# Kernel tuning notes

Hardware: AMD Instinct MI355X
Metric: run time of the kernel (lower is better)

Reference implementation:

```python
import jax, jax.numpy as jnp
import numpy as np
from jax import lax

B, C_IN, H, W = 32, 2048, 14, 14
C_MID = 1024
EPS = 1e-5


def _bn(x, gamma, beta, mean, var):
    # eval-mode batchnorm over channel axis 1 of NCHW
    inv = gamma / jnp.sqrt(var + EPS)
    return x * inv[None, :, None, None] + (beta - mean * inv)[None, :, None, None]


def setup_inputs() -> dict:
    key = jax.random.key(0)
    ks = jax.random.split(key, 16)
    x = jax.random.normal(ks[0], (B, C_IN, H, W), jnp.float32)
    # conv1: 3x3, 2048 -> 1024, xavier-normal init
    std1 = np.sqrt(2.0 / (C_IN * 9 + C_MID * 9)).astype(np.float32)
    w1 = jax.random.normal(ks[1], (C_MID, C_IN, 3, 3), jnp.float32) * std1
    b1 = jnp.zeros((C_MID,), jnp.float32)
    bn1_gamma = 1.0 + 0.1 * jax.random.normal(ks[2], (C_MID,), jnp.float32)
    bn1_beta = 0.1 * jax.random.normal(ks[3], (C_MID,), jnp.float32)
    bn1_mean = 0.1 * jax.random.normal(ks[4], (C_MID,), jnp.float32)
    bn1_var = jax.random.uniform(ks[5], (C_MID,), jnp.float32, 0.5, 1.5)
    # selectLayer: 1x1, 1024 -> 18 (stored as [out, in])
    std_s = np.sqrt(2.0 / (C_MID + 18)).astype(np.float32)
    w_sel = jax.random.normal(ks[6], (18, C_MID), jnp.float32) * std_s
    b_sel = jnp.zeros((18,), jnp.float32)
    # boxLayer: 1x1, 1024 -> 36, uniform(-5, 5) init
    w_box = jax.random.uniform(ks[7], (36, C_MID), jnp.float32, -5.0, 5.0)
    b_box = jnp.zeros((36,), jnp.float32)
    bnb_gamma = 1.0 + 0.1 * jax.random.normal(ks[8], (36,), jnp.float32)
    bnb_beta = 0.1 * jax.random.normal(ks[9], (36,), jnp.float32)
    bnb_mean = 0.1 * jax.random.normal(ks[10], (36,), jnp.float32)
    bnb_var = jax.random.uniform(ks[11], (36,), jnp.float32, 0.5, 1.5)
    return {
        'x': x, 'w1': w1, 'b1': b1,
        'bn1_gamma': bn1_gamma, 'bn1_beta': bn1_beta, 'bn1_mean': bn1_mean, 'bn1_var': bn1_var,
        'w_sel': w_sel, 'b_sel': b_sel,
        'w_box': w_box, 'b_box': b_box,
        'bnb_gamma': bnb_gamma, 'bnb_beta': bnb_beta, 'bnb_mean': bnb_mean, 'bnb_var': bnb_var,
    }


def reference(x, w1, b1, bn1_gamma, bn1_beta, bn1_mean, bn1_var,
              w_sel, b_sel, w_box, b_box,
              bnb_gamma, bnb_beta, bnb_mean, bnb_var):
    n = x.shape[0]
    # conv1 + BN + ReLU (3x3, padding=1)
    h = lax.conv_general_dilated(x, w1, (1, 1), 'SAME',
                                 dimension_numbers=('NCHW', 'OIHW', 'NCHW'))
    h = h + b1[None, :, None, None]
    h = jax.nn.relu(_bn(h, bn1_gamma, bn1_beta, bn1_mean, bn1_var))
    # selectLayer: 1x1 conv + ReLU -> [n, 18, H, W]
    score = jnp.einsum('nchw,oc->nohw', h, w_sel) + b_sel[None, :, None, None]
    score = jax.nn.relu(score)
    # boxLayer: 1x1 conv + BN + ReLU -> [n, 36, H, W]
    box = jnp.einsum('nchw,oc->nohw', h, w_box) + b_box[None, :, None, None]
    box = jax.nn.relu(_bn(box, bnb_gamma, bnb_beta, bnb_mean, bnb_var))
    # permute NCHW -> NHWC, reshape to anchors
    box = jnp.transpose(box, (0, 2, 3, 1)).reshape(n, -1, 4) * 419.0  # [n, 1764, 4]
    score = jnp.transpose(score, (0, 2, 3, 1)).reshape(n, -1, 2)      # [n, 1764, 2]
    score = jax.nn.softmax(score, axis=-1)
    return score, box
```

## Files before the change

kernel.cpp:

```cpp
#include <hip/hip_runtime.h>
#include <hip/hip_bf16.h>
#include <math.h>

#define CIN   2048
#define CMID  1024
#define NB    32
#define HWSP  196
#define NPOS  6272
#define WELEM 2097152
#define NST64 144

typedef __attribute__((ext_vector_type(4))) float f32x4;
typedef __attribute__((ext_vector_type(8))) short short8;
typedef __attribute__((ext_vector_type(4))) float float4v;

typedef const __attribute__((address_space(1))) unsigned int* as1_u32p;
typedef __attribute__((address_space(3))) unsigned int* as3_u32p;

__device__ __forceinline__ void gload_lds16(const void* g, void* l) {
  __builtin_amdgcn_global_load_lds((as1_u32p)g, (as3_u32p)l, 16, 0, 0);
}

__global__ __launch_bounds__(256) void pack_w(
    const float* __restrict__ w1, const float* __restrict__ b1,
    const float* __restrict__ g1, const float* __restrict__ be1,
    const float* __restrict__ mu1, const float* __restrict__ va1,
    const float* __restrict__ wsel, const float* __restrict__ wbox,
    __hip_bfloat16* __restrict__ Wp, float* __restrict__ inv1,
    float* __restrict__ add1, float* __restrict__ Wh)
{
  __shared__ float lw[2304];
  const int gid0 = blockIdx.x * 256;
  const float4v* src4 = (const float4v*)(w1 + (long)gid0 * 9);
  float4v* l4 = (float4v*)lw;
  #pragma unroll
  for (int i = 0; i < 3; ++i) {
    int idx = i * 256 + threadIdx.x;
    if (idx < 576) l4[idx] = src4[idx];
  }
  __syncthreads();
  const int gid = gid0 + threadIdx.x;
  float v[9];
  #pragma unroll
  for (int k = 0; k < 9; ++k) v[k] = lw[threadIdx.x * 9 + k];
  #pragma unroll
  for (int k = 0; k < 9; ++k)
    Wp[(long)k * WELEM + gid] = __float2bfloat16(v[k]);

  if (gid < CMID) {
    float iv = g1[gid] / sqrtf(va1[gid] + 1e-5f);
    inv1[gid] = iv;
    add1[gid] = b1[gid] * iv + be1[gid] - mu1[gid] * iv;
  }
  if (gid < CMID * 54) {
    int co = gid / 54, o = gid % 54;
    Wh[gid] = (o < 18) ? wsel[o * CMID + co] : wbox[(o - 18) * CMID + co];
  }
}

__global__ __launch_bounds__(256) void pack_x(
    const float* __restrict__ x, __hip_bfloat16* __restrict__ Xp)
{
  __shared__ __hip_bfloat16 lx[64 * HWSP];
  const int n = blockIdx.x;
  const int cc = blockIdx.y;
  const int ci0 = cc * 64;
  const float* src = x + ((long)n * CIN + ci0) * HWSP;
  for (int i = threadIdx.x; i < 64 * HWSP; i += 256)
    lx[i] = __float2bfloat16(src[i]);
  __syncthreads();
  const int ci = threadIdx.x & 63;
  const int pq = threadIdx.x >> 6;
  __hip_bfloat16* dst = Xp + (long)n * 256 * CIN + ci0 + ci;
  const __hip_bfloat16 z = __float2bfloat16(0.f);
  #pragma unroll
  for (int k = 0; k < 64; ++k) {
    int pos = k * 4 + pq;
    int y = pos >> 4, xx = pos & 15;
    __hip_bfloat16 v = z;
    if (y >= 1 && y <= 14 && xx >= 1 && xx <= 14)
      v = lx[ci * HWSP + (y - 1) * 14 + (xx - 1)];
    dst[(long)pos * CIN] = v;
  }
}

__global__ __launch_bounds__(256, 2) void conv_mfma(
    const __hip_bfloat16* __restrict__ Wp,
    const __hip_bfloat16* __restrict__ Xp,
    __hip_bfloat16* __restrict__ hout0,
    __hip_bfloat16* __restrict__ hout1)
{
  __shared__ char smem[2 * 32768];

  const int t = threadIdx.x;
  const int bx = blockIdx.x;
  const int r  = bx & 7;
  const int q  = bx >> 3;
  const int kidx = q >> 3;
  int mtile = q & 7;
  int ntile;
  if (kidx < 6) {
    ntile = r + 8 * kidx;
  } else {
    if (r != (q & 7)) return;
    ntile = 48;
  }
  const int z = blockIdx.y;
  const int lane = t & 63;
  const int wv = t >> 6;
  const int wr2 = wv >> 1;
  const int wc2 = wv & 1;

  const int srow = t >> 2;
  const int swb = ((t & 3) << 4) ^ ((srow & 6) << 3);

  const long arowbase = (long)(mtile * 128 + srow) * CIN + (swb >> 1);

  long bbase[2];
  #pragma unroll
  for (int i = 0; i < 2; ++i) {
    int jj = ntile * 128 + srow + 64 * i;
    int n0 = jj / HWSP, p0 = jj % HWSP;
    int hh = p0 / 14, ww = p0 % 14;
    bbase[i] = (long)(n0 * 256 + hh * 16 + ww) * CIN + (swb >> 1);
  }

  const int fr = lane & 15;
  const int ksl = lane >> 4;
  const int kgsw = ((ksl << 4) ^ ((fr & 6) << 3));

  f32x4 acc[4][4] = {};
  short8 a_[4], b_[4];

  const int g0 = z * NST64;

  #define STAGE_A(gv, bi) do {                                                  \
    int g_ = (gv);                                                              \
    int kt_ = g_ >> 5;                                                          \
    int ck_ = (g_ & 31) << 6;                                                   \
    char* d_ = smem + (bi) * 32768;                                             \
    const __hip_bfloat16* ap_ = Wp + (long)kt_ * WELEM + arowbase + ck_;        \
    _Pragma("unroll")                                                           \
    for (int h_ = 0; h_ < 2; ++h_)                                              \
      _Pragma("unroll")                                                         \
      for (int i_ = 0; i_ < 2; ++i_)                                            \
        gload_lds16(ap_ + h_ * 32 + (long)i_ * 64 * CIN,                        \
                    d_ + h_ * 8192 + i_ * 4096 + t * 16);                       \
  } while (0)

  #define STAGE_B(gv, bi) do {                                                  \
    int g_ = (gv);                                                              \
    int kt_ = g_ >> 5;                                                          \
    int ck_ = (g_ & 31) << 6;                                                   \
    int kh_ = (kt_ * 11) >> 5;                                                  \
    int kw_ = kt_ - kh_ * 3;                                                    \
    char* d_ = smem + (bi) * 32768 + 16384;                                     \
    long boff_ = (long)(kh_ * 16 + kw_) * CIN + ck_;                            \
    _Pragma("unroll")                                                           \
    for (int h_ = 0; h_ < 2; ++h_)                                              \
      _Pragma("unroll")                                                         \
      for (int i_ = 0; i_ < 2; ++i_)                                            \
        gload_lds16(Xp + bbase[i_] + boff_ + h_ * 32,                           \
                    d_ + h_ * 8192 + i_ * 4096 + t * 16);                       \
  } while (0)

  #define READ_H(bi, h) do {                                                    \
    const char* cb_ = smem + (bi) * 32768 + (h) * 8192;                         \
    _Pragma("unroll")                                                           \
    for (int i = 0; i < 4; ++i)                                                 \
      a_[i] = *(const short8*)(cb_ + (wr2 * 64 + i * 16 + fr) * 64 + kgsw);     \
    _Pragma("unroll")                                                           \
    for (int i = 0; i < 4; ++i)                                                 \
      b_[i] = *(const short8*)(cb_ + 16384 + (wc2 * 64 + i * 16 + fr) * 64 + kgsw); \
  } while (0)

  #define MFMA_H() do {                                                         \
    __builtin_amdgcn_s_setprio(1);                                              \
    _Pragma("unroll")                                                           \
    for (int m = 0; m < 4; ++m)                                                 \
      _Pragma("unroll")                                                         \
      for (int n = 0; n < 4; ++n)                                               \
        acc[m][n] = __builtin_amdgcn_mfma_f32_16x16x32_bf16(a_[m], b_[n], acc[m][n], 0, 0, 0); \
    __builtin_amdgcn_s_setprio(0);                                              \
  } while (0)

  #define WAITV4() asm volatile("s_waitcnt vmcnt(4)" ::: "memory")
  #define WAITV0() asm volatile("s_waitcnt vmcnt(0)" ::: "memory")
  #define BAR() do { asm volatile("" ::: "memory");                             \
                     __builtin_amdgcn_s_barrier();                              \
                     asm volatile("" ::: "memory"); } while (0)

  STAGE_A(g0 + 0, 0);
  STAGE_B(g0 + 0, 0);

  for (int s = 0; s < NST64 - 1; ++s) {
    const int c = s & 1, n = c ^ 1;
    STAGE_A(g0 + s + 1, n);
    WAITV4();
    BAR();
    READ_H(c, 0);
    MFMA_H();
    STAGE_B(g0 + s + 1, n);
    READ_H(c, 1);
    BAR();
    MFMA_H();
  }
  {
    const int c = (NST64 - 1) & 1;
    WAITV0(); BAR();
    READ_H(c, 0);
    MFMA_H();
    READ_H(c, 1);
    MFMA_H();
  }

  __hip_bfloat16* dsth = z ? hout1 : hout0;
  const int rg = ksl * 4;
  #pragma unroll
  for (int m = 0; m < 4; ++m) {
    const int co0 = mtile * 128 + wr2 * 64 + m * 16 + rg;
    #pragma unroll
    for (int r_ = 0; r_ < 4; ++r_) {
      const int co = co0 + r_;
      #pragma unroll
      for (int n = 0; n < 4; ++n) {
        const int j = ntile * 128 + wc2 * 64 + n * 16 + fr;
        dsth[(long)co * NPOS + j] = __float2bfloat16(acc[m][n][r_]);
      }
    }
  }
  #undef STAGE_A
  #undef STAGE_B
  #undef READ_H
  #undef MFMA_H
  #undef WAITV4
  #undef WAITV0
  #undef BAR
}

__global__ __launch_bounds__(256) void head_fused(
    const __hip_bfloat16* __restrict__ h0, const __hip_bfloat16* __restrict__ h1,
    const float* __restrict__ Wh,
    const float* __restrict__ inv1, const float* __restrict__ add1,
    const float* __restrict__ bsel, const float* __restrict__ bbox,
    const float* __restrict__ gb, const float* __restrict__ beb,
    const float* __restrict__ mub, const float* __restrict__ vab,
    float* __restrict__ out)
{
  __shared__ float red[4 * 64 * 54];
  const int t = threadIdx.x;
  const int jl = t & 63;
  const int cg = __builtin_amdgcn_readfirstlane(t >> 6);
  const int j0 = blockIdx.x * 64;
  const int j = j0 + jl;

  float acc[54];
  #pragma unroll
  for (int o = 0; o < 54; ++o) acc[o] = 0.f;

  const __hip_bfloat16* hp0 = h0 + (long)(cg * 256) * NPOS + j;
  const __hip_bfloat16* hp1 = h1 + (long)(cg * 256) * NPOS + j;
  const float* wp = Wh + cg * 256 * 54;
  const float* ivp = inv1 + cg * 256;
  const float* adp = add1 + cg * 256;
  for (int i = 0; i < 256; ++i) {
    float hv = __bfloat162float(hp0[(long)i * NPOS]) + __bfloat162float(hp1[(long)i * NPOS]);
    hv = fmaxf(hv * ivp[i] + adp[i], 0.f);
    const float* wr_ = wp + i * 54;
    #pragma unroll
    for (int o = 0; o < 54; ++o) acc[o] += hv * wr_[o];
  }
  #pragma unroll
  for (int o = 0; o < 54; ++o) red[(cg * 64 + jl) * 54 + o] = acc[o];
  __syncthreads();

  for (int idx = t; idx < 576; idx += 256) {
    int jj = idx / 9, pr = idx % 9;
    float s0 = bsel[2 * pr], s1 = bsel[2 * pr + 1];
    #pragma unroll
    for (int c = 0; c < 4; ++c) {
      s0 += red[(c * 64 + jj) * 54 + 2 * pr];
      s1 += red[(c * 64 + jj) * 54 + 2 * pr + 1];
    }
    s0 = fmaxf(s0, 0.f); s1 = fmaxf(s1, 0.f);
    float mx = fmaxf(s0, s1);
    float e0 = expf(s0 - mx), e1 = expf(s1 - mx);
    float inv = 1.f / (e0 + e1);
    int jg = j0 + jj;
    int nn = jg / HWSP, p = jg % HWSP;
    long off = ((long)nn * 1764 + p * 9 + pr) * 2;
    out[off] = e0 * inv;
    out[off + 1] = e1 * inv;
  }

  float* outb = out + (long)NB * 1764 * 2;
  for (int idx = t; idx < 2304; idx += 256) {
    int jj = idx / 36, o = idx % 36;
    float v = bbox[o];
    #pragma unroll
    for (int c = 0; c < 4; ++c) v += red[(c * 64 + jj) * 54 + 18 + o];
    float iv = gb[o] / sqrtf(vab[o] + 1e-5f);
    v = v * iv + (beb[o] - mub[o] * iv);
    v = fmaxf(v, 0.f) * 419.f;
    int jg = j0 + jj;
    int nn = jg / HWSP, p = jg % HWSP;
    outb[((long)nn * 1764 + p * 9 + (o >> 2)) * 4 + (o & 3)] = v;
  }
}

extern "C" void kernel_launch(void* const* d_in, const int* in_sizes, int n_in,
                              void* d_out, int out_size, void* d_ws, size_t ws_size,
                              hipStream_t stream) {
  const float* x    = (const float*)d_in[0];
  const float* w1   = (const float*)d_in[1];
  const float* b1   = (const float*)d_in[2];
  const float* g1   = (const float*)d_in[3];
  const float* be1  = (const float*)d_in[4];
  const float* mu1  = (const float*)d_in[5];
  const float* va1  = (const float*)d_in[6];
  const float* wsel = (const float*)d_in[7];
  const float* bsel = (const float*)d_in[8];
  const float* wbox = (const float*)d_in[9];
  const float* bbox = (const float*)d_in[10];
  const float* gb   = (const float*)d_in[11];
  const float* beb  = (const float*)d_in[12];
  const float* mub  = (const float*)d_in[13];
  const float* vab  = (const float*)d_in[14];

  char* ws = (char*)d_ws;
  __hip_bfloat16* Wp = (__hip_bfloat16*)(ws);
  __hip_bfloat16* Xp = (__hip_bfloat16*)(ws + 37748736);
  __hip_bfloat16* hb0 = (__hip_bfloat16*)(ws + 71303168);
  __hip_bfloat16* hb1 = (__hip_bfloat16*)(ws + 84148224);
  float* inv1        = (float*)(ws + 96993280);
  float* add1        = (float*)(ws + 96997376);
  float* Wh          = (float*)(ws + 97001472);

  hipLaunchKernelGGL(pack_w, dim3(8192), dim3(256), 0, stream,
                     w1, b1, g1, be1, mu1, va1, wsel, wbox, Wp, inv1, add1, Wh);
  hipLaunchKernelGGL(pack_x, dim3(32, 32), dim3(256), 0, stream, x, Xp);
  hipLaunchKernelGGL(conv_mfma, dim3(448, 2), dim3(256), 0, stream,
                     Wp, Xp, hb0, hb1);
  hipLaunchKernelGGL(head_fused, dim3(98), dim3(256), 0, stream,
                     hb0, hb1, Wh, inv1, add1, bsel, bbox, gb, beb, mub, vab, (float*)d_out);
}
```

Before: 403.2 us.

## Merge weight and input pack kernels; read both K-halves from LDS before MFMAs

Combines pack_w and pack_x into one launch that dispatches on block index, removing a kernel launch and the gap between the two packing passes. In the conv main loop, both halves of the LDS tile are read into separate register sets before the first MFMA batch, so the second batch runs without waiting on LDS reads. This raises VGPR use (two extra short8[4] sets), which could hurt occupancy under launch_bounds(256,2). The merged pack kernel also reserves the larger shared buffer for every block.

```diff
diff --git a/kernel.cpp b/kernel.cpp
--- a/kernel.cpp
+++ b/kernel.cpp
@@ -21,66 +21,68 @@
   __builtin_amdgcn_global_load_lds((as1_u32p)g, (as3_u32p)l, 16, 0, 0);
 }
 
-__global__ __launch_bounds__(256) void pack_w(
+__global__ __launch_bounds__(256) void pack_all(
     const float* __restrict__ w1, const float* __restrict__ b1,
     const float* __restrict__ g1, const float* __restrict__ be1,
     const float* __restrict__ mu1, const float* __restrict__ va1,
     const float* __restrict__ wsel, const float* __restrict__ wbox,
+    const float* __restrict__ x,
     __hip_bfloat16* __restrict__ Wp, float* __restrict__ inv1,
-    float* __restrict__ add1, float* __restrict__ Wh)
+    float* __restrict__ add1, float* __restrict__ Wh,
+    __hip_bfloat16* __restrict__ Xp)
 {
-  __shared__ float lw[2304];
-  const int gid0 = blockIdx.x * 256;
-  const float4v* src4 = (const float4v*)(w1 + (long)gid0 * 9);
-  float4v* l4 = (float4v*)lw;
-  #pragma unroll
-  for (int i = 0; i < 3; ++i) {
-    int idx = i * 256 + threadIdx.x;
-    if (idx < 576) l4[idx] = src4[idx];
-  }
-  __syncthreads();
-  const int gid = gid0 + threadIdx.x;
-  float v[9];
-  #pragma unroll
-  for (int k = 0; k < 9; ++k) v[k] = lw[threadIdx.x * 9 + k];
-  #pragma unroll
-  for (int k = 0; k < 9; ++k)
-    Wp[(long)k * WELEM + gid] = __float2bfloat16(v[k]);
-
-  if (gid < CMID) {
-    float iv = g1[gid] / sqrtf(va1[gid] + 1e-5f);
-    inv1[gid] = iv;
-    add1[gid] = b1[gid] * iv + be1[gid] - mu1[gid] * iv;
-  }
-  if (gid < CMID * 54) {
-    int co = gid / 54, o = gid % 54;
-    Wh[gid] = (o < 18) ? wsel[o * CMID + co] : wbox[(o - 18) * CMID + co];
-  }
-}
-
-__global__ __launch_bounds__(256) void pack_x(
-    const float* __restrict__ x, __hip_bfloat16* __restrict__ Xp)
-{
-  __shared__ __hip_bfloat16 lx[64 * HWSP];
-  const int n = blockIdx.x;
-  const int cc = blockIdx.y;
-  const int ci0 = cc * 64;
-  const float* src = x + ((long)n * CIN + ci0) * HWSP;
-  for (int i = threadIdx.x; i < 64 * HWSP; i += 256)
-    lx[i] = __float2bfloat16(src[i]);
-  __syncthreads();
-  const int ci = threadIdx.x & 63;
-  const int pq = threadIdx.x >> 6;
-  __hip_bfloat16* dst = Xp + (long)n * 256 * CIN + ci0 + ci;
-  const __hip_bfloat16 z = __float2bfloat16(0.f);
-  #pragma unroll
-  for (int k = 0; k < 64; ++k) {
-    int pos = k * 4 + pq;
-    int y = pos >> 4, xx = pos & 15;
-    __hip_bfloat16 v = z;
-    if (y >= 1 && y <= 14 && xx >= 1 && xx <= 14)
-      v = lx[ci * HWSP + (y - 1) * 14 + (xx - 1)];
-    dst[(long)pos * CIN] = v;
+  __shared__ char shm[25088];
+  if (blockIdx.x < 8192) {
+    float* lw = (float*)shm;
+    const int gid0 = blockIdx.x * 256;
+    const float4v* src4 = (const float4v*)(w1 + (long)gid0 * 9);
+    float4v* l4 = (float4v*)lw;
+    #pragma unroll
+    for (int i = 0; i < 3; ++i) {
+      int idx = i * 256 + threadIdx.x;
+      if (idx < 576) l4[idx] = src4[idx];
+    }
+    __syncthreads();
+    const int gid = gid0 + threadIdx.x;
+    float v[9];
+    #pragma unroll
+    for (int k = 0; k < 9; ++k) v[k] = lw[threadIdx.x * 9 + k];
+    #pragma unroll
+    for (int k = 0; k < 9; ++k)
+      Wp[(long)k * WELEM + gid] = __float2bfloat16(v[k]);
+
+    if (gid < CMID) {
+      float iv = g1[gid] / sqrtf(va1[gid] + 1e-5f);
+      inv1[gid] = iv;
+      add1[gid] = b1[gid] * iv + be1[gid] - mu1[gid] * iv;
+    }
+    if (gid < CMID * 54) {
+      int co = gid / 54, o = gid % 54;
+      Wh[gid] = (o < 18) ? wsel[o * CMID + co] : wbox[(o - 18) * CMID + co];
+    }
+  } else {
+    __hip_bfloat16* lx = (__hip_bfloat16*)shm;
+    const int b = blockIdx.x - 8192;
+    const int n = b >> 5;
+    const int cc = b & 31;
+    const int ci0 = cc * 64;
+    const float* src = x + ((long)n * CIN + ci0) * HWSP;
+    for (int i = threadIdx.x; i < 64 * HWSP; i += 256)
+      lx[i] = __float2bfloat16(src[i]);
+    __syncthreads();
+    const int ci = threadIdx.x & 63;
+    const int pq = threadIdx.x >> 6;
+    __hip_bfloat16* dst = Xp + (long)n * 256 * CIN + ci0 + ci;
+    const __hip_bfloat16 z = __float2bfloat16(0.f);
+    #pragma unroll
+    for (int k = 0; k < 64; ++k) {
+      int pos = k * 4 + pq;
+      int y = pos >> 4, xx = pos & 15;
+      __hip_bfloat16 v = z;
+      if (y >= 1 && y <= 14 && xx >= 1 && xx <= 14)
+        v = lx[ci * HWSP + (y - 1) * 14 + (xx - 1)];
+      dst[(long)pos * CIN] = v;
+    }
   }
 }
 
@@ -130,7 +132,7 @@
   const int kgsw = ((ksl << 4) ^ ((fr & 6) << 3));
 
   f32x4 acc[4][4] = {};
-  short8 a_[4], b_[4];
+  short8 aA[4], bA[4], aB[4], bB[4];
 
   const int g0 = z * NST64;
 
@@ -164,23 +166,30 @@
                     d_ + h_ * 8192 + i_ * 4096 + t * 16);                       \
   } while (0)
 
-  #define READ_H(bi, h) do {                                                    \
-    const char* cb_ = smem + (bi) * 32768 + (h) * 8192;                         \
+  #define READ_H2(bi) do {                                                      \
+    const char* c0_ = smem + (bi) * 32768;                                      \
+    const char* c1_ = c0_ + 8192;                                               \
     _Pragma("unroll")                                                           \
     for (int i = 0; i < 4; ++i)                                                 \
-      a_[i] = *(const short8*)(cb_ + (wr2 * 64 + i * 16 + fr) * 64 + kgsw);     \
+      aA[i] = *(const short8*)(c0_ + (wr2 * 64 + i * 16 + fr) * 64 + kgsw);     \
     _Pragma("unroll")                                                           \
     for (int i = 0; i < 4; ++i)                                                 \
-      b_[i] = *(const short8*)(cb_ + 16384 + (wc2 * 64 + i * 16 + fr) * 64 + kgsw); \
+      bA[i] = *(const short8*)(c0_ + 16384 + (wc2 * 64 + i * 16 + fr) * 64 + kgsw); \
+    _Pragma("unroll")                                                           \
+    for (int i = 0; i < 4; ++i)                                                 \
+      aB[i] = *(const short8*)(c1_ + (wr2 * 64 + i * 16 + fr) * 64 + kgsw);     \
+    _Pragma("unroll")                                                           \
+    for (int i = 0; i < 4; ++i)                                                 \
+      bB[i] = *(const short8*)(c1_ + 16384 + (wc2 * 64 + i * 16 + fr) * 64 + kgsw); \
   } while (0)
 
-  #define MFMA_H() do {                                                         \
+  #define MFMA16(av, bv) do {                                                   \
     __builtin_amdgcn_s_setprio(1);                                              \
     _Pragma("unroll")                                                           \
     for (int m = 0; m < 4; ++m)                                                 \
       _Pragma("unroll")                                                         \
       for (int n = 0; n < 4; ++n)                                               \
-        acc[m][n] = __builtin_amdgcn_mfma_f32_16x16x32_bf16(a_[m], b_[n], acc[m][n], 0, 0, 0); \
+        acc[m][n] = __builtin_amdgcn_mfma_f32_16x16x32_bf16(av[m], bv[n], acc[m][n], 0, 0, 0); \
     __builtin_amdgcn_s_setprio(0);                                              \
   } while (0)
 
@@ -198,20 +207,18 @@
     STAGE_A(g0 + s + 1, n);
     WAITV4();
     BAR();
-    READ_H(c, 0);
-    MFMA_H();
+    READ_H2(c);
+    MFMA16(aA, bA);
     STAGE_B(g0 + s + 1, n);
-    READ_H(c, 1);
     BAR();
-    MFMA_H();
+    MFMA16(aB, bB);
   }
   {
     const int c = (NST64 - 1) & 1;
     WAITV0(); BAR();
-    READ_H(c, 0);
-    MFMA_H();
-    READ_H(c, 1);
-    MFMA_H();
+    READ_H2(c);
+    MFMA16(aA, bA);
+    MFMA16(aB, bB);
   }
 
   __hip_bfloat16* dsth = z ? hout1 : hout0;
@@ -231,8 +238,8 @@
   }
   #undef STAGE_A
   #undef STAGE_B
-  #undef READ_H
-  #undef MFMA_H
+  #undef READ_H2
+  #undef MFMA16
   #undef WAITV4
   #undef WAITV0
   #undef BAR
@@ -336,9 +343,8 @@
   float* add1        = (float*)(ws + 96997376);
   float* Wh          = (float*)(ws + 97001472);
 
-  hipLaunchKernelGGL(pack_w, dim3(8192), dim3(256), 0, stream,
-                     w1, b1, g1, be1, mu1, va1, wsel, wbox, Wp, inv1, add1, Wh);
-  hipLaunchKernelGGL(pack_x, dim3(32, 32), dim3(256), 0, stream, x, Xp);
+  hipLaunchKernelGGL(pack_all, dim3(9216), dim3(256), 0, stream,
+                     w1, b1, g1, be1, mu1, va1, wsel, wbox, x, Wp, inv1, add1, Wh, Xp);
   hipLaunchKernelGGL(conv_mfma, dim3(448, 2), dim3(256), 0, stream,
                      Wp, Xp, hb0, hb1);
   hipLaunchKernelGGL(head_fused, dim3(98), dim3(256), 0, stream,
```

Result: slower. 413.2 us (+2.5%).
